# Optimization experiments

Hardware: AMD Instinct MI355X
Metric: run time of the kernel (lower is better)

## Reference

```python
import jax, jax.numpy as jnp
import numpy as np

B = 32768          # batch
SEQ, F = 128, 8    # input_seq_len_samples, num_features
D = SEQ * F        # flattened input dim = 1024
E = 16             # num_experts
H1 = 256           # expert hidden
H2 = H1 // 2       # 128
GH = 128           # gating hidden


def _init_linear(key, fan_in, shape_w, shape_b):
    # torch nn.Linear default: U(-1/sqrt(fan_in), 1/sqrt(fan_in))
    kw, kb = jax.random.split(key)
    lim = 1.0 / np.sqrt(fan_in)
    W = jax.random.uniform(kw, shape_w, jnp.float32, -lim, lim)
    b = jax.random.uniform(kb, shape_b, jnp.float32, -lim, lim)
    return W, b


def setup_inputs() -> dict:
    key = jax.random.key(0)
    ks = jax.random.split(key, 6)
    x = jax.random.normal(ks[0], (B, SEQ, F), jnp.float32)
    # stacked expert weights: [E, in, out] layout
    W1, b1 = _init_linear(ks[1], D, (E, D, H1), (E, H1))
    W2, b2 = _init_linear(ks[2], H1, (E, H1, H2), (E, H2))
    W3, b3 = _init_linear(ks[3], H2, (E, H2, 1), (E, 1))
    Wg1, bg1 = _init_linear(ks[4], D, (D, GH), (GH,))
    Wg2, bg2 = _init_linear(ks[5], GH, (GH, E), (E,))
    return {"x": x, "W1": W1, "b1": b1, "W2": W2, "b2": b2,
            "W3": W3, "b3": b3, "Wg1": Wg1, "bg1": bg1,
            "Wg2": Wg2, "bg2": bg2}


def reference(x, W1, b1, W2, b2, W3, b3, Wg1, bg1, Wg2, bg2):
    bsz = x.shape[0]
    flat_x = x.reshape(bsz, -1)                      # [B, D]
    # gating network
    g = jax.nn.relu(flat_x @ Wg1 + bg1)              # [B, GH]
    gating_logits = g @ Wg2 + bg2                    # [B, E]
    gating_weights = jax.nn.softmax(gating_logits, axis=1)
    # all experts as one batched GEMM stack
    h = jax.nn.relu(jnp.einsum('bd,edh->beh', flat_x, W1) + b1)   # [B,E,H1]
    h = jax.nn.relu(jnp.einsum('beh,ehk->bek', h, W2) + b2)       # [B,E,H2]
    expert_outputs = jnp.einsum('bek,eko->beo', h, W3) + b3       # [B,E,1]
    final_output = jnp.sum(gating_weights[:, :, None] * expert_outputs, axis=1)  # [B,1]
    return final_output, gating_weights
```

## Files before the change

kernel.cpp:

```cpp
#include <hip/hip_runtime.h>
#include <stdint.h>
#include <stddef.h>

typedef short bf16x8 __attribute__((ext_vector_type(8)));
typedef float f32x4 __attribute__((ext_vector_type(4)));

__device__ __forceinline__ unsigned short bf16rn(float f){
  unsigned int u = __builtin_bit_cast(unsigned int, f);
  u += 0x7fffu + ((u >> 16) & 1u);
  return (unsigned short)(u >> 16);
}

__device__ __forceinline__ void gll16(const void* gsrc, void* ldst){
  __builtin_amdgcn_global_load_lds((const __attribute__((address_space(1))) unsigned int*)gsrc,
                                   (__attribute__((address_space(3))) unsigned int*)ldst,
                                   16, 0, 0);
}

__device__ __forceinline__ void barfence(){
  asm volatile("" ::: "memory");
  __builtin_amdgcn_s_barrier();
  asm volatile("" ::: "memory");
}

__global__ __launch_bounds__(256) void k_cvt_x(const float* __restrict__ x,
                                               unsigned short* __restrict__ xb, long n){
  long i = ((long)blockIdx.x * blockDim.x + threadIdx.x) * 8;
  if (i >= n) return;
  const float4* p = (const float4*)(x + i);
  float4 a = p[0], b = p[1];
  union { unsigned short h[8]; uint4 u; } r;
  r.h[0]=bf16rn(a.x); r.h[1]=bf16rn(a.y); r.h[2]=bf16rn(a.z); r.h[3]=bf16rn(a.w);
  r.h[4]=bf16rn(b.x); r.h[5]=bf16rn(b.y); r.h[6]=bf16rn(b.z); r.h[7]=bf16rn(b.w);
  *(uint4*)(xb + i) = r.u;
}

__global__ __launch_bounds__(256) void k_cvt_w(const float* __restrict__ src,
                                               unsigned short* __restrict__ dst,
                                               int K, int N){
  __shared__ float t[32][33];
  int e = blockIdx.z, k0 = blockIdx.x * 32, n0 = blockIdx.y * 32;
  const float* s = src + (size_t)e * K * N;
  unsigned short* d = dst + (size_t)e * N * K;
  int tx = threadIdx.x, ty = threadIdx.y;
  #pragma unroll
  for (int j = 0; j < 4; j++)
    t[ty + j*8][tx] = s[(size_t)(k0 + ty + j*8) * N + n0 + tx];
  __syncthreads();
  #pragma unroll
  for (int j = 0; j < 4; j++){
    int n = ty + j*8;
    d[(size_t)(n0 + n) * K + k0 + tx] = bf16rn(t[tx][n]);
  }
}

__global__ __launch_bounds__(128) void k_gating(const unsigned short* __restrict__ xb,
                                                const unsigned short* __restrict__ wg1t,
                                                const float* __restrict__ bg1,
                                                const float* __restrict__ wg2,
                                                const float* __restrict__ bg2,
                                                float* __restrict__ gout, int chunk_base){
  __shared__ unsigned short As[32*64];
  __shared__ unsigned short Bs[128*64];
  __shared__ float gl[32][129];
  const int t = threadIdx.x, wid = t >> 6, l = t & 63;
  const int m0 = blockIdx.x * 32;
  const int jb = l & 7, rsub = l >> 3;
  f32x4 acc[2][4];
  #pragma unroll
  for (int i=0;i<2;i++)
    #pragma unroll
    for (int j=0;j<4;j++) acc[i][j] = (f32x4)0.f;

  for (int kt = 0; kt < 16; kt++){
    int k0 = kt * 64;
    #pragma unroll
    for (int i = 0; i < 2; i++){
      int idx = wid*2 + i; int row = idx*8 + rsub;
      gll16(xb + (size_t)(m0 + row)*1024 + k0 + ((jb ^ (row & 7)) << 3), As + idx*512);
    }
    #pragma unroll
    for (int i = 0; i < 8; i++){
      int idx = wid*8 + i; int row = idx*8 + rsub;
      gll16(wg1t + (size_t)row*1024 + k0 + ((jb ^ (row & 7)) << 3), Bs + idx*512);
    }
    __syncthreads();
    #pragma unroll
    for (int ks = 0; ks < 2; ks++){
      int blk = ks*4 + (l >> 4);
      bf16x8 a[2], b[4];
      #pragma unroll
      for (int fi = 0; fi < 2; fi++){
        int r = fi*16 + (l & 15);
        a[fi] = *(const bf16x8*)(As + r*64 + ((blk ^ (r & 7)) << 3));
      }
      #pragma unroll
      for (int fj = 0; fj < 4; fj++){
        int r = wid*64 + fj*16 + (l & 15);
        b[fj] = *(const bf16x8*)(Bs + r*64 + ((blk ^ (r & 7)) << 3));
      }
      #pragma unroll
      for (int fi = 0; fi < 2; fi++)
        #pragma unroll
        for (int fj = 0; fj < 4; fj++)
          acc[fi][fj] = __builtin_amdgcn_mfma_f32_16x16x32_bf16(a[fi], b[fj], acc[fi][fj], 0, 0, 0);
    }
    __syncthreads();
  }
  #pragma unroll
  for (int fi = 0; fi < 2; fi++)
    #pragma unroll
    for (int fj = 0; fj < 4; fj++){
      int c = wid*64 + fj*16 + (l & 15);
      float bv = bg1[c];
      #pragma unroll
      for (int r = 0; r < 4; r++){
        int row = fi*16 + (l >> 4)*4 + r;
        float v = acc[fi][fj][r] + bv;
        gl[row][c] = v > 0.f ? v : 0.f;
      }
    }
  __syncthreads();
  if (t < 32){
    float le[16];
    #pragma unroll
    for (int e = 0; e < 16; e++) le[e] = bg2[e];
    for (int k = 0; k < 128; k++){
      float g = gl[t][k];
      const float* w = wg2 + k*16;
      #pragma unroll
      for (int e = 0; e < 16; e++) le[e] += g * w[e];
    }
    float m = le[0];
    #pragma unroll
    for (int e = 1; e < 16; e++) m = fmaxf(m, le[e]);
    float s = 0.f;
    #pragma unroll
    for (int e = 0; e < 16; e++){ le[e] = __expf(le[e] - m); s += le[e]; }
    float inv = 1.f / s;
    float4* o = (float4*)(gout + (size_t)(chunk_base + m0 + t)*16);
    #pragma unroll
    for (int q = 0; q < 4; q++)
      o[q] = make_float4(le[4*q]*inv, le[4*q+1]*inv, le[4*q+2]*inv, le[4*q+3]*inv);
  }
}

template<int I0, int J0>
__device__ __forceinline__ void mfma_quad(const bf16x8 (&A)[4][2], const bf16x8 (&Bv)[2][2],
                                          f32x4 (&acc)[8][4]){
  #pragma unroll
  for (int fi = 0; fi < 4; ++fi)
    #pragma unroll
    for (int ks = 0; ks < 2; ++ks){
      acc[I0+fi][J0]   = __builtin_amdgcn_mfma_f32_16x16x32_bf16(A[fi][ks], Bv[0][ks], acc[I0+fi][J0],   0,0,0);
      acc[I0+fi][J0+1] = __builtin_amdgcn_mfma_f32_16x16x32_bf16(A[fi][ks], Bv[1][ks], acc[I0+fi][J0+1], 0,0,0);
    }
}

__global__ __launch_bounds__(512, 2) void k_stage1_8ph(const unsigned short* __restrict__ xb,
                                                       const unsigned short* __restrict__ w1t,
                                                       const float* __restrict__ b1,
                                                       unsigned short* __restrict__ h1,
                                                       int chunkB){
  extern __shared__ __align__(16) char smem[];
  const int t = threadIdx.x;
  const int wid = t >> 6, l = t & 63;
  const int wrow = wid >> 2, wcol = wid & 3;
  const int l3 = l >> 3, l7 = l & 7, l15 = l & 15, l4 = l >> 4;

  const int bid = blockIdx.x;
  const int wg = (bid & 7) * ((int)gridDim.x >> 3) + (bid >> 3);
  const int mt = wg >> 4, e = wg & 15;
  const int m0 = mt * 256, n0 = e * 256;

  auto STAGE = [&](int isB, int p, int h, int kt){
    const unsigned short* gb = isB ? (w1t + (size_t)(n0 + h*128) * 1024)
                                   : (xb  + (size_t)(m0 + h*128) * 1024);
    char* dbase = smem + ((p << 16) | (isB << 15) | (h << 14));
    #pragma unroll
    for (int j = 0; j < 2; j++){
      int r = j*64 + wid*8 + l3;
      size_t src = (size_t)r * 1024 + (size_t)kt*64 + (size_t)((l7 ^ (r & 7)) << 3);
      gll16(gb + src, dbase + j*8192 + wid*1024);
    }
  };
  auto LDA = [&](int p, int qm, int fi, int ks) -> bf16x8 {
    int row = qm*64 + fi*16 + l15;
    int kb = (((ks << 2) | l4) ^ (row & 7)) << 4;
    return *(const bf16x8*)(smem + (p << 16) + (wrow << 14) + row*128 + kb);
  };
  auto LDB = [&](int p, int qn, int fj, int ks) -> bf16x8 {
    int row = (wcol & 1)*64 + qn*32 + fj*16 + l15;
    int kb = (((ks << 2) | l4) ^ (row & 7)) << 4;
    return *(const bf16x8*)(smem + (p << 16) + 32768 + ((wcol >> 1) << 14) + row*128 + kb);
  };

  f32x4 acc[8][4];
  #pragma unroll
  for (int i = 0; i < 8; i++)
    #pragma unroll
    for (int j = 0; j < 4; j++) acc[i][j] = (f32x4)0.f;

  bf16x8 a0[4][2], a1[4][2], b0[2][2], b1v[2][2];

  STAGE(0,0,0,0); STAGE(1,0,0,0); STAGE(0,0,1,0); STAGE(1,0,1,0);
  STAGE(1,1,0,1); STAGE(0,1,0,1);
  asm volatile("s_waitcnt vmcnt(4)" ::: "memory");
  barfence();

  for (int it = 0; it < 8; ++it){
    const int t0 = 2*it, k1 = t0 + 1;
    int c2 = t0 + 2, c3 = t0 + 3;
    if (c2 > 15) c2 = 14;
    if (c3 > 15) c3 = 14;

    #pragma unroll
    for (int fi = 0; fi < 4; ++fi){ a0[fi][0] = LDA(0,0,fi,0); a0[fi][1] = LDA(0,0,fi,1); }
    #pragma unroll
    for (int fj = 0; fj < 2; ++fj){ b0[fj][0] = LDB(0,0,fj,0); b0[fj][1] = LDB(0,0,fj,1); }
    STAGE(1,1,1,k1);
    barfence();
    __builtin_amdgcn_s_setprio(1);
    mfma_quad<0,0>(a0, b0, acc);
    __builtin_amdgcn_s_setprio(0);
    barfence();

    #pragma unroll
    for (int fj = 0; fj < 2; ++fj){ b1v[fj][0] = LDB(0,1,fj,0); b1v[fj][1] = LDB(0,1,fj,1); }
    STAGE(0,1,1,k1);
    barfence();
    __builtin_amdgcn_s_setprio(1);
    mfma_quad<0,2>(a0, b1v, acc);
    __builtin_amdgcn_s_setprio(0);
    barfence();

    #pragma unroll
    for (int fi = 0; fi < 4; ++fi){ a1[fi][0] = LDA(0,1,fi,0); a1[fi][1] = LDA(0,1,fi,1); }
    STAGE(1,0,0,c2);
    barfence();
    __builtin_amdgcn_s_setprio(1);
    mfma_quad<4,2>(a1, b1v, acc);
    __builtin_amdgcn_s_setprio(0);
    barfence();

    STAGE(0,0,0,c2);
    barfence();
    __builtin_amdgcn_s_setprio(1);
    mfma_quad<4,0>(a1, b0, acc);
    __builtin_amdgcn_s_setprio(0);
    asm volatile("s_waitcnt vmcnt(4)" ::: "memory");
    barfence();

    #pragma unroll
    for (int fi = 0; fi < 4; ++fi){ a0[fi][0] = LDA(1,0,fi,0); a0[fi][1] = LDA(1,0,fi,1); }
    #pragma unroll
    for (int fj = 0; fj < 2; ++fj){ b0[fj][0] = LDB(1,0,fj,0); b0[fj][1] = LDB(1,0,fj,1); }
    STAGE(1,0,1,c2);
    barfence();
    __builtin_amdgcn_s_setprio(1);
    mfma_quad<0,0>(a0, b0, acc);
    __builtin_amdgcn_s_setprio(0);
    barfence();

    #pragma unroll
    for (int fj = 0; fj < 2; ++fj){ b1v[fj][0] = LDB(1,1,fj,0); b1v[fj][1] = LDB(1,1,fj,1); }
    STAGE(0,0,1,c2);
    barfence();
    __builtin_amdgcn_s_setprio(1);
    mfma_quad<0,2>(a0, b1v, acc);
    __builtin_amdgcn_s_setprio(0);
    barfence();

    #pragma unroll
    for (int fi = 0; fi < 4; ++fi){ a1[fi][0] = LDA(1,1,fi,0); a1[fi][1] = LDA(1,1,fi,1); }
    STAGE(1,1,0,c3);
    barfence();
    __builtin_amdgcn_s_setprio(1);
    mfma_quad<4,2>(a1, b1v, acc);
    __builtin_amdgcn_s_setprio(0);
    barfence();

    STAGE(0,1,0,c3);
    barfence();
    __builtin_amdgcn_s_setprio(1);
    mfma_quad<4,0>(a1, b0, acc);
    __builtin_amdgcn_s_setprio(0);
    asm volatile("s_waitcnt vmcnt(4)" ::: "memory");
    barfence();
  }

  const int rb = m0 + wrow*128;
  #pragma unroll
  for (int fi = 0; fi < 8; ++fi)
    #pragma unroll
    for (int fj = 0; fj < 4; ++fj){
      const int c = wcol*64 + fj*16 + l15;
      const float bv = b1[e*256 + c];
      #pragma unroll
      for (int r = 0; r < 4; ++r){
        const int row = rb + fi*16 + l4*4 + r;
        float v = acc[fi][fj][r] + bv;
        v = v > 0.f ? v : 0.f;
        h1[((size_t)e*chunkB + row)*256 + c] = bf16rn(v);
      }
    }
}

__global__ __launch_bounds__(512) void k_stage2a(const unsigned short* __restrict__ h1,
                                                 const unsigned short* __restrict__ w2t,
                                                 const float* __restrict__ b2,
                                                 const float* __restrict__ w3,
                                                 const float* __restrict__ b3,
                                                 float* __restrict__ outE,
                                                 int mtiles, int chunkB){
  __shared__ unsigned short As[256*64];
  __shared__ unsigned short Bs[128*64];
  __shared__ float red[256][2];
  const int t = threadIdx.x, wid = t >> 6, l = t & 63;
  const int e = blockIdx.x / mtiles, mt = blockIdx.x % mtiles;
  const int m0 = mt*256;
  const int jb = l & 7, rsub = l >> 3;
  const int wrow = wid >> 1, wc = wid & 1;
  const unsigned short* asrc = h1 + ((size_t)e*chunkB + m0)*256;
  const unsigned short* bsrc = w2t + (size_t)e*(128*256);
  f32x4 acc[4][4];
  #pragma unroll
  for (int i=0;i<4;i++)
    #pragma unroll
    for (int j=0;j<4;j++) acc[i][j] = (f32x4)0.f;

  for (int kt = 0; kt < 4; kt++){
    int k0 = kt*64;
    #pragma unroll
    for (int i = 0; i < 4; i++){
      int idx = wid*4 + i; int row = idx*8 + rsub;
      gll16(asrc + (size_t)row*256 + k0 + ((jb ^ (row & 7)) << 3), As + idx*512);
    }
    #pragma unroll
    for (int i = 0; i < 2; i++){
      int idx = wid*2 + i; int row = idx*8 + rsub;
      gll16(bsrc + (size_t)row*256 + k0 + ((jb ^ (row & 7)) << 3), Bs + idx*512);
    }
    __syncthreads();
    #pragma unroll
    for (int ks = 0; ks < 2; ks++){
      int blk = ks*4 + (l >> 4);
      bf16x8 a[4], b[4];
      #pragma unroll
      for (int fi = 0; fi < 4; fi++){
        int r = wrow*64 + fi*16 + (l & 15);
        a[fi] = *(const bf16x8*)(As + r*64 + ((blk ^ (r & 7)) << 3));
      }
      #pragma unroll
      for (int fj = 0; fj < 4; fj++){
        int r = wc*64 + fj*16 + (l & 15);
        b[fj] = *(const bf16x8*)(Bs + r*64 + ((blk ^ (r & 7)) << 3));
      }
      #pragma unroll
      for (int fi = 0; fi < 4; fi++)
        #pragma unroll
        for (int fj = 0; fj < 4; fj++)
          acc[fi][fj] = __builtin_amdgcn_mfma_f32_16x16x32_bf16(a[fi], b[fj], acc[fi][fj], 0, 0, 0);
    }
    __syncthreads();
  }
  float w3v[4], b2v[4];
  #pragma unroll
  for (int fj = 0; fj < 4; fj++){
    int c = wc*64 + fj*16 + (l & 15);
    w3v[fj] = w3[e*128 + c];
    b2v[fj] = b2[e*128 + c];
  }
  #pragma unroll
  for (int fi = 0; fi < 4; fi++){
    #pragma unroll
    for (int r = 0; r < 4; r++){
      float s = 0.f;
      #pragma unroll
      for (int fj = 0; fj < 4; fj++){
        float v = acc[fi][fj][r] + b2v[fj];
        v = v > 0.f ? v : 0.f;
        s += v * w3v[fj];
      }
      s += __shfl_xor(s, 1); s += __shfl_xor(s, 2);
      s += __shfl_xor(s, 4); s += __shfl_xor(s, 8);
      if ((l & 15) == 0){
        int row = wrow*64 + fi*16 + (l >> 4)*4 + r;
        red[row][wc] = s;
      }
    }
  }
  __syncthreads();
  if (t < 256)
    outE[(size_t)e*chunkB + m0 + t] = red[t][0] + red[t][1] + b3[e];
}

__global__ __launch_bounds__(256) void k_stage2b(const float* __restrict__ outE,
                                                 float* __restrict__ dout,
                                                 int chunk_base, int chunkB, int Btot){
  int row = blockIdx.x*256 + threadIdx.x;
  int rowg = chunk_base + row;
  const float* g = dout + Btot + (size_t)rowg*16;
  float s = 0.f;
  #pragma unroll
  for (int e = 0; e < 16; e++) s += g[e] * outE[(size_t)e*chunkB + row];
  dout[rowg] = s;
}

extern "C" void kernel_launch(void* const* d_in, const int* in_sizes, int n_in,
                              void* d_out, int out_size, void* d_ws, size_t ws_size,
                              hipStream_t stream){
  const float* x   = (const float*)d_in[0];
  const float* W1  = (const float*)d_in[1];
  const float* b1  = (const float*)d_in[2];
  const float* W2  = (const float*)d_in[3];
  const float* b2  = (const float*)d_in[4];
  const float* W3  = (const float*)d_in[5];
  const float* b3  = (const float*)d_in[6];
  const float* Wg1 = (const float*)d_in[7];
  const float* bg1 = (const float*)d_in[8];
  const float* Wg2 = (const float*)d_in[9];
  const float* bg2 = (const float*)d_in[10];
  float* out = (float*)d_out;

  const int B = in_sizes[0] / 1024;

  char* ws = (char*)d_ws;
  size_t off = 0;
  auto alloc = [&](size_t bytes){ size_t p = off; off = (off + bytes + 255) & ~(size_t)255; return p; };
  size_t o_w1t  = alloc((size_t)16*256*1024*2);
  size_t o_w2t  = alloc((size_t)16*128*256*2);
  size_t o_wg1t = alloc((size_t)128*1024*2);
  size_t fixed = off;

  const int cands[6] = {1, 2, 4, 8, 16, 32};
  int nc = 32;
  for (int i = 0; i < 6; i++){
    size_t cB = (size_t)B / cands[i];
    if (fixed + cB*10304 + 4096 <= ws_size){ nc = cands[i]; break; }
  }
  int chunkB = B / nc;

  size_t o_xb = alloc((size_t)chunkB*1024*2);
  size_t o_h1 = alloc((size_t)chunkB*16*256*2);
  size_t o_oe = alloc((size_t)chunkB*16*4);

  unsigned short* w1t  = (unsigned short*)(ws + o_w1t);
  unsigned short* w2t  = (unsigned short*)(ws + o_w2t);
  unsigned short* wg1t = (unsigned short*)(ws + o_wg1t);
  unsigned short* xb   = (unsigned short*)(ws + o_xb);
  unsigned short* h1   = (unsigned short*)(ws + o_h1);
  float*          oE   = (float*)(ws + o_oe);

  hipFuncSetAttribute(reinterpret_cast<const void*>(k_stage1_8ph),
                      hipFuncAttributeMaxDynamicSharedMemorySize, 131072);

  k_cvt_w<<<dim3(32, 8, 16), dim3(32, 8), 0, stream>>>(W1, w1t, 1024, 256);
  k_cvt_w<<<dim3(8, 4, 16),  dim3(32, 8), 0, stream>>>(W2, w2t, 256, 128);
  k_cvt_w<<<dim3(32, 4, 1),  dim3(32, 8), 0, stream>>>(Wg1, wg1t, 1024, 128);

  for (int c = 0; c < nc; c++){
    int cb = c * chunkB;
    k_cvt_x<<<chunkB/2, 256, 0, stream>>>(x + (size_t)cb*1024, xb, (long)chunkB*1024);
    k_gating<<<chunkB/32, 128, 0, stream>>>(xb, wg1t, bg1, Wg2, bg2, out + B, cb);
    k_stage1_8ph<<<chunkB/16, 512, 131072, stream>>>(xb, w1t, b1, h1, chunkB);
    k_stage2a<<<16*(chunkB/256), 512, 0, stream>>>(h1, w2t, b2, W3, b3, oE, chunkB/256, chunkB);
    k_stage2b<<<chunkB/256, 256, 0, stream>>>(oE, out, cb, chunkB, B);
  }
}
```

Before: 439.0 us.

## Fuse expert layer-1 GEMM with layer-2/3 by keeping hidden tile in LDS

Merges the stage-1 kernel and the stage-2a kernel into one. After the W1 GEMM, the ReLU'd bf16 hidden tile is written into LDS with an XOR swizzle instead of to global memory. The W2 GEMM and the W3 dot product then run in the same block, with double-buffered W2 staging in extra LDS. This removes the large h1 global write and read and one launch per chunk. It also shrinks the workspace per row, which allows larger chunks. The cost is 160KB of dynamic LDS per block and a serialized second GEMM phase that cannot overlap with other blocks' stage-1 work.

New measurement: 368.8 us. 1.19x faster.

```diff
diff --git a/kernel.cpp b/kernel.cpp
--- a/kernel.cpp
+++ b/kernel.cpp
@@ -157,11 +157,15 @@
     }
 }
 
-__global__ __launch_bounds__(512, 2) void k_stage1_8ph(const unsigned short* __restrict__ xb,
-                                                       const unsigned short* __restrict__ w1t,
-                                                       const float* __restrict__ b1,
-                                                       unsigned short* __restrict__ h1,
-                                                       int chunkB){
+__global__ __launch_bounds__(512, 2) void k_fused(const unsigned short* __restrict__ xb,
+                                                  const unsigned short* __restrict__ w1t,
+                                                  const float* __restrict__ b1,
+                                                  const unsigned short* __restrict__ w2t,
+                                                  const float* __restrict__ b2,
+                                                  const float* __restrict__ w3,
+                                                  const float* __restrict__ b3,
+                                                  float* __restrict__ outE,
+                                                  int chunkB){
   extern __shared__ __align__(16) char smem[];
   const int t = threadIdx.x;
   const int wid = t >> 6, l = t & 63;
@@ -289,110 +293,108 @@
     barfence();
   }
 
-  const int rb = m0 + wrow*128;
-  #pragma unroll
-  for (int fi = 0; fi < 8; ++fi)
-    #pragma unroll
-    for (int fj = 0; fj < 4; ++fj){
-      const int c = wcol*64 + fj*16 + l15;
-      const float bv = b1[e*256 + c];
-      #pragma unroll
-      for (int r = 0; r < 4; ++r){
-        const int row = rb + fi*16 + l4*4 + r;
-        float v = acc[fi][fj][r] + bv;
-        v = v > 0.f ? v : 0.f;
-        h1[((size_t)e*chunkB + row)*256 + c] = bf16rn(v);
-      }
-    }
-}
-
-__global__ __launch_bounds__(512) void k_stage2a(const unsigned short* __restrict__ h1,
-                                                 const unsigned short* __restrict__ w2t,
-                                                 const float* __restrict__ b2,
-                                                 const float* __restrict__ w3,
-                                                 const float* __restrict__ b3,
-                                                 float* __restrict__ outE,
-                                                 int mtiles, int chunkB){
-  __shared__ unsigned short As[256*64];
-  __shared__ unsigned short Bs[128*64];
-  __shared__ float red[256][2];
-  const int t = threadIdx.x, wid = t >> 6, l = t & 63;
-  const int e = blockIdx.x / mtiles, mt = blockIdx.x % mtiles;
-  const int m0 = mt*256;
-  const int jb = l & 7, rsub = l >> 3;
-  const int wrow = wid >> 1, wc = wid & 1;
-  const unsigned short* asrc = h1 + ((size_t)e*chunkB + m0)*256;
-  const unsigned short* bsrc = w2t + (size_t)e*(128*256);
-  f32x4 acc[4][4];
-  #pragma unroll
-  for (int i=0;i<4;i++)
-    #pragma unroll
-    for (int j=0;j<4;j++) acc[i][j] = (f32x4)0.f;
-
-  for (int kt = 0; kt < 4; kt++){
-    int k0 = kt*64;
-    #pragma unroll
-    for (int i = 0; i < 4; i++){
-      int idx = wid*4 + i; int row = idx*8 + rsub;
-      gll16(asrc + (size_t)row*256 + k0 + ((jb ^ (row & 7)) << 3), As + idx*512);
-    }
-    #pragma unroll
-    for (int i = 0; i < 2; i++){
-      int idx = wid*2 + i; int row = idx*8 + rsub;
-      gll16(bsrc + (size_t)row*256 + k0 + ((jb ^ (row & 7)) << 3), Bs + idx*512);
-    }
-    __syncthreads();
-    #pragma unroll
-    for (int ks = 0; ks < 2; ks++){
-      int blk = ks*4 + (l >> 4);
-      bf16x8 a[4], b[4];
-      #pragma unroll
-      for (int fi = 0; fi < 4; fi++){
-        int r = wrow*64 + fi*16 + (l & 15);
-        a[fi] = *(const bf16x8*)(As + r*64 + ((blk ^ (r & 7)) << 3));
-      }
-      #pragma unroll
-      for (int fj = 0; fj < 4; fj++){
-        int r = wc*64 + fj*16 + (l & 15);
-        b[fj] = *(const bf16x8*)(Bs + r*64 + ((blk ^ (r & 7)) << 3));
-      }
-      #pragma unroll
-      for (int fi = 0; fi < 4; fi++)
+  __syncthreads();
+
+  {
+    float bv[4];
+    #pragma unroll
+    for (int fj = 0; fj < 4; ++fj) bv[fj] = b1[e*256 + wcol*64 + fj*16 + l15];
+    #pragma unroll
+    for (int fi = 0; fi < 8; ++fi)
+      #pragma unroll
+      for (int fj = 0; fj < 4; ++fj){
+        const int col = wcol*64 + fj*16 + l15;
         #pragma unroll
-        for (int fj = 0; fj < 4; fj++)
-          acc[fi][fj] = __builtin_amdgcn_mfma_f32_16x16x32_bf16(a[fi], b[fj], acc[fi][fj], 0, 0, 0);
-    }
-    __syncthreads();
-  }
+        for (int r = 0; r < 4; ++r){
+          const int row = wrow*128 + fi*16 + l4*4 + r;
+          float v = acc[fi][fj][r] + bv[fj];
+          v = v > 0.f ? v : 0.f;
+          *(unsigned short*)(smem + row*512 + (((col >> 3) ^ (row & 7)) << 4) + ((col & 7) << 1)) = bf16rn(v);
+        }
+      }
+  }
+
+  const unsigned short* w2e = w2t + (size_t)e*(128*256);
+  auto STAGE_W2 = [&](int c, int q){
+    char* dbase = smem + 131072 + q*16384;
+    #pragma unroll
+    for (int j = 0; j < 2; j++){
+      int r = j*64 + wid*8 + l3;
+      size_t src = (size_t)r*256 + (size_t)c*64 + (size_t)((l7 ^ (r & 7)) << 3);
+      gll16(w2e + src, dbase + j*8192 + wid*1024);
+    }
+  };
+  STAGE_W2(0, 0);
+  __syncthreads();
+
+  const int wr2 = wid >> 1, wc2 = wid & 1;
+  f32x4 acc2[4][4];
+  #pragma unroll
+  for (int i = 0; i < 4; i++)
+    #pragma unroll
+    for (int j = 0; j < 4; j++) acc2[i][j] = (f32x4)0.f;
+
   float w3v[4], b2v[4];
   #pragma unroll
-  for (int fj = 0; fj < 4; fj++){
-    int c = wc*64 + fj*16 + (l & 15);
+  for (int fj = 0; fj < 4; ++fj){
+    int c = wc2*64 + fj*16 + l15;
     w3v[fj] = w3[e*128 + c];
     b2v[fj] = b2[e*128 + c];
   }
-  #pragma unroll
-  for (int fi = 0; fi < 4; fi++){
-    #pragma unroll
-    for (int r = 0; r < 4; r++){
+
+  for (int c = 0; c < 4; ++c){
+    if (c < 3) STAGE_W2(c+1, (c+1)&1);
+    bf16x8 a2[4][2], bb[4][2];
+    #pragma unroll
+    for (int fi = 0; fi < 4; ++fi)
+      #pragma unroll
+      for (int ks = 0; ks < 2; ++ks){
+        int row = wr2*64 + fi*16 + l15;
+        int sl = (c*8 + ks*4 + l4) ^ (row & 7);
+        a2[fi][ks] = *(const bf16x8*)(smem + row*512 + (sl << 4));
+      }
+    #pragma unroll
+    for (int fj = 0; fj < 4; ++fj)
+      #pragma unroll
+      for (int ks = 0; ks < 2; ++ks){
+        int n = wc2*64 + fj*16 + l15;
+        int sl = (ks*4 + l4) ^ (n & 7);
+        bb[fj][ks] = *(const bf16x8*)(smem + 131072 + (c&1)*16384 + n*128 + (sl << 4));
+      }
+    __builtin_amdgcn_s_setprio(1);
+    #pragma unroll
+    for (int fi = 0; fi < 4; ++fi)
+      #pragma unroll
+      for (int fj = 0; fj < 4; ++fj)
+        #pragma unroll
+        for (int ks = 0; ks < 2; ++ks)
+          acc2[fi][fj] = __builtin_amdgcn_mfma_f32_16x16x32_bf16(a2[fi][ks], bb[fj][ks], acc2[fi][fj], 0, 0, 0);
+    __builtin_amdgcn_s_setprio(0);
+    __syncthreads();
+  }
+
+  float* red = (float*)(smem + 131072);
+  #pragma unroll
+  for (int fi = 0; fi < 4; ++fi)
+    #pragma unroll
+    for (int r = 0; r < 4; ++r){
       float s = 0.f;
       #pragma unroll
-      for (int fj = 0; fj < 4; fj++){
-        float v = acc[fi][fj][r] + b2v[fj];
+      for (int fj = 0; fj < 4; ++fj){
+        float v = acc2[fi][fj][r] + b2v[fj];
         v = v > 0.f ? v : 0.f;
         s += v * w3v[fj];
       }
       s += __shfl_xor(s, 1); s += __shfl_xor(s, 2);
       s += __shfl_xor(s, 4); s += __shfl_xor(s, 8);
-      if ((l & 15) == 0){
-        int row = wrow*64 + fi*16 + (l >> 4)*4 + r;
-        red[row][wc] = s;
-      }
-    }
-  }
+      if (l15 == 0){
+        int row = wr2*64 + fi*16 + l4*4 + r;
+        red[row*2 + wc2] = s;
+      }
+    }
   __syncthreads();
   if (t < 256)
-    outE[(size_t)e*chunkB + m0 + t] = red[t][0] + red[t][1] + b3[e];
+    outE[(size_t)e*chunkB + m0 + t] = red[t*2 + 0] + red[t*2 + 1] + b3[e];
 }
 
 __global__ __launch_bounds__(256) void k_stage2b(const float* __restrict__ outE,
@@ -437,23 +439,21 @@
   int nc = 32;
   for (int i = 0; i < 6; i++){
     size_t cB = (size_t)B / cands[i];
-    if (fixed + cB*10304 + 4096 <= ws_size){ nc = cands[i]; break; }
+    if (fixed + cB*2112 + 4096 <= ws_size){ nc = cands[i]; break; }
   }
   int chunkB = B / nc;
 
   size_t o_xb = alloc((size_t)chunkB*1024*2);
-  size_t o_h1 = alloc((size_t)chunkB*16*256*2);
   size_t o_oe = alloc((size_t)chunkB*16*4);
 
   unsigned short* w1t  = (unsigned short*)(ws + o_w1t);
   unsigned short* w2t  = (unsigned short*)(ws + o_w2t);
   unsigned short* wg1t = (unsigned short*)(ws + o_wg1t);
   unsigned short* xb   = (unsigned short*)(ws + o_xb);
-  unsigned short* h1   = (unsigned short*)(ws + o_h1);
   float*          oE   = (float*)(ws + o_oe);
 
-  hipFuncSetAttribute(reinterpret_cast<const void*>(k_stage1_8ph),
-                      hipFuncAttributeMaxDynamicSharedMemorySize, 131072);
+  hipFuncSetAttribute(reinterpret_cast<const void*>(k_fused),
+                      hipFuncAttributeMaxDynamicSharedMemorySize, 163840);
 
   k_cvt_w<<<dim3(32, 8, 16), dim3(32, 8), 0, stream>>>(W1, w1t, 1024, 256);
   k_cvt_w<<<dim3(8, 4, 16),  dim3(32, 8), 0, stream>>>(W2, w2t, 256, 128);
@@ -463,8 +463,7 @@
     int cb = c * chunkB;
     k_cvt_x<<<chunkB/2, 256, 0, stream>>>(x + (size_t)cb*1024, xb, (long)chunkB*1024);
     k_gating<<<chunkB/32, 128, 0, stream>>>(xb, wg1t, bg1, Wg2, bg2, out + B, cb);
-    k_stage1_8ph<<<chunkB/16, 512, 131072, stream>>>(xb, w1t, b1, h1, chunkB);
-    k_stage2a<<<16*(chunkB/256), 512, 0, stream>>>(h1, w2t, b2, W3, b3, oE, chunkB/256, chunkB);
+    k_fused<<<chunkB/16, 512, 163840, stream>>>(xb, w1t, b1, w2t, b2, W3, b3, oE, chunkB);
     k_stage2b<<<chunkB/256, 256, 0, stream>>>(oE, out, cb, chunkB, B);
   }
 }
```
